# Performance work log

Hardware: AMD Instinct MI355X
Metric: run time of the kernel (lower is better)

## Reference

```python
import jax, jax.numpy as jnp
import numpy as np
import math

N, K, IFZ, AH, AF, QP, VP = 4096, 24, 256, 12, 48, 4, 8


def _rope(x, ang):
    # x: (..., AF), ang: (..., AF//2) rotary angles
    xr = x.reshape(x.shape[:-1] + (AF // 2, 2))
    c, s = jnp.cos(ang), jnp.sin(ang)
    xe, xo = xr[..., 0], xr[..., 1]
    out = jnp.stack([xe * c - xo * s, xe * s + xo * c], axis=-1)
    return out.reshape(x.shape)


def _affine_mul(R, t, vecs):
    # R: (N,3,3), t: (N,3), vecs: (N, ..., 3) -> rigid transform, broadcast over middle dims
    out = jnp.einsum('nij,n...j->n...i', R, vecs)
    return out + t.reshape((t.shape[0],) + (1,) * (vecs.ndim - 2) + (3,))


def setup_inputs():
    key = jax.random.key(0)
    ks = jax.random.split(key, 16)
    sc = 1.0 / math.sqrt(IFZ)
    return {
        'x1': jax.random.normal(ks[0], (N, IFZ), jnp.float32),
        'x2': jax.random.normal(ks[1], (N, K, IFZ // 2), jnp.float32),
        'affines': jax.random.normal(ks[2], (N, 3, 4), jnp.float32),
        'pos_emb': jax.random.normal(ks[3], (N, AF // 2), jnp.float32),
        'edge_index': jax.random.randint(ks[4], (N, K), 0, N),
        'Wq1': jax.random.normal(ks[5], (IFZ, AH * AF), jnp.float32) * sc,
        'Wk1': jax.random.normal(ks[6], (IFZ, AH * AF), jnp.float32) * sc,
        'Wv1': jax.random.normal(ks[7], (IFZ, AH * AF), jnp.float32) * sc,
        'Wq2': jax.random.normal(ks[8], (IFZ, AH * QP * 3), jnp.float32) * sc,
        'Wk2': jax.random.normal(ks[9], (IFZ, AH * QP * 3), jnp.float32) * sc,
        'Wv2': jax.random.normal(ks[10], (IFZ, AH * VP * 3), jnp.float32) * sc,
        'Wbia': jax.random.normal(ks[11], (IFZ // 2, AH), jnp.float32) * (1.0 / math.sqrt(IFZ // 2)),
        'gamma': 1.1 * jnp.ones((1, 1, AH), jnp.float32),
        'Wback': jax.random.normal(ks[12], (AH * AF + AH * (IFZ // 2) + AH * VP * 3 + AH * VP, IFZ), jnp.float32) * 0.02,
        'bback': jnp.zeros((IFZ,), jnp.float32),
        'ln_g': jnp.ones((IFZ,), jnp.float32),
        'ln_b': jnp.zeros((IFZ,), jnp.float32),
    }


def _forward(x1, x2, affines, pos_emb, Wq1, Wk1, Wv1, Wq2, Wk2, Wv2, Wbia, gamma, Wback, bback, ln_g, ln_b, edge_index):
    n = x1.shape[0]
    q1 = (x1 @ Wq1).reshape(n, AH, AF)
    k1 = (x1 @ Wk1).reshape(n, AH, AF)[edge_index]            # (N,K,AH,AF) irregular gather
    q1 = _rope(q1, pos_emb[:, None, :])                       # rotate query by own position
    k1 = _rope(k1, pos_emb[edge_index][:, :, None, :])        # rotate keys by source position
    v1 = (x1 @ Wv1).reshape(n, AH, AF)[edge_index]            # (N,K,AH,AF)
    q2 = (x1 @ Wq2).reshape(n, 1, AH, QP, 3)
    k2 = (x1 @ Wk2).reshape(n, AH, QP, 3)[edge_index]         # (N,K,AH,QP,3)
    v2 = (x1 @ Wv2).reshape(n, AH, VP, 3)
    bias = x2 @ Wbia                                          # (N,K,AH)
    R, t = affines[:, :, :3], affines[:, :, 3]
    wc = math.sqrt(2.0 / (9.0 * QP))
    wl = math.sqrt(1.0 / 3.0)
    s1 = jnp.einsum('nai,nkai->nka', q1, k1) / math.sqrt(AF) + bias
    d = _affine_mul(R, t, q2) - _affine_mul(R, t, k2)         # (N,K,AH,QP,3) point distances
    s2 = -jnp.sum(jnp.square(d), axis=(-1, -2))               # (N,K,AH)
    scores = wl * (s1 + 0.1 * wc * gamma * s2)
    w = jax.nn.softmax(scores, axis=1)                        # softmax over K neighbors
    out1 = jnp.einsum('nka,nkai->nai', w, v1)                 # (N,AH,AF)
    out2 = jnp.einsum('nka,nki->nai', w, x2)                  # (N,AH,IFZ//2)
    v2g = _affine_mul(R, t, v2)[edge_index]                   # transform then gather: (N,K,AH,VP,3)
    oipa = jnp.einsum('nka,nkavd->navd', w, v2g)              # (N,AH,VP,3)
    Rinv = jnp.swapaxes(R, -1, -2)
    tinv = -jnp.einsum('nij,nj->ni', Rinv, t)
    oipa = _affine_mul(Rinv, tinv, oipa)                      # back to local frame
    onorm = jnp.sqrt(jnp.sum(jnp.square(oipa), axis=-1))      # (N,AH,VP)
    cat = jnp.concatenate([out1.reshape(n, -1), out2.reshape(n, -1), oipa.reshape(n, -1), onorm.reshape(n, -1)], axis=1)
    out = cat @ Wback + bback
    h = math.sqrt(2.0) * x1 + out                             # residual with sqrt(2) scale
    mu = jnp.mean(h, axis=-1, keepdims=True)
    var = jnp.var(h, axis=-1, keepdims=True)
    return (h - mu) / jnp.sqrt(var + 1e-5) * ln_g + ln_b


def reference(x1, x2, affines, pos_emb, edge_index, Wq1, Wk1, Wv1, Wq2, Wk2, Wv2, Wbia, gamma, Wback, bback, ln_g, ln_b):
    return _forward(x1, x2, affines, pos_emb, Wq1, Wk1, Wv1, Wq2, Wk2, Wv2, Wbia, gamma, Wback, bback, ln_g, ln_b, edge_index)
```

## Files before the change

kernel.cpp:

```cpp
#include <hip/hip_runtime.h>
#include <hip/hip_bf16.h>
#include <math.h>

#define NN   4096
#define KK   24
#define IFZ  256
#define AH   12
#define AF   48
#define QP   4
#define VP   8

#define TAB_STRIDE 2304
#define Q1OFF 0
#define K1OFF 576
#define V1OFF 1152
#define Q2OFF 1728
#define K2OFF 1872
#define V2OFF 2016

#define CAT_STRIDE 2496
#define CAT_OUT2 576
#define CAT_OIPA 2112
#define CAT_ONRM 2400

#define SPLITK 6

#define WL      0.57735026918962576f
#define C2      0.023570226039551584f
#define RSQRT48 0.14433756729740643f

__global__ __launch_bounds__(256) void pack_w(
    const float* __restrict__ Wq1, const float* __restrict__ Wk1,
    const float* __restrict__ Wv1, const float* __restrict__ Wq2,
    const float* __restrict__ Wk2, const float* __restrict__ Wv2,
    float* __restrict__ packW)
{
    int idx = blockIdx.x * 256 + threadIdx.x;
    int i = idx / TAB_STRIDE;
    int j = idx % TAB_STRIDE;
    float v;
    if (j < 576)       v = Wq1[i*576 + j];
    else if (j < 1152) v = Wk1[i*576 + (j-576)];
    else if (j < 1728) v = Wv1[i*576 + (j-1152)];
    else if (j < 1872) v = Wq2[i*144 + (j-1728)];
    else if (j < 2016) v = Wk2[i*144 + (j-1872)];
    else               v = Wv2[i*288 + (j-2016)];
    packW[idx] = v;
}

__global__ __launch_bounds__(256) void gemm1(
    const float* __restrict__ A, const float* __restrict__ B,
    float* __restrict__ C, int M, int Nc, int Kc)
{
    __shared__ __align__(16) float sA[32][68];
    __shared__ __align__(16) float sB[32][68];
    int bx = blockIdx.x;
    int by = blockIdx.y;
    int tid = threadIdx.x;
    int tx = tid & 15, ty = tid >> 4;
    float acc[4][4] = {};
    for (int k0 = 0; k0 < Kc; k0 += 32) {
        #pragma unroll
        for (int l = 0; l < 2; ++l) {
            int idx = tid + l*256;
            int m = idx >> 3, k4 = (idx & 7) * 4;
            float4 av = *(const float4*)&A[(size_t)(by*64 + m)*Kc + k0 + k4];
            sA[k4+0][m] = av.x; sA[k4+1][m] = av.y;
            sA[k4+2][m] = av.z; sA[k4+3][m] = av.w;
        }
        #pragma unroll
        for (int l = 0; l < 2; ++l) {
            int idx = tid + l*256;
            int kk = idx >> 4, j = (idx & 15) * 4;
            *(float4*)&sB[kk][j] = *(const float4*)&B[(size_t)(k0 + kk)*Nc + bx*64 + j];
        }
        __syncthreads();
        #pragma unroll
        for (int kk = 0; kk < 32; ++kk) {
            float4 a4 = *(const float4*)&sA[kk][ty*4];
            float4 b4 = *(const float4*)&sB[kk][tx*4];
            float a[4] = {a4.x, a4.y, a4.z, a4.w};
            float b[4] = {b4.x, b4.y, b4.z, b4.w};
            #pragma unroll
            for (int u = 0; u < 4; ++u)
                #pragma unroll
                for (int v = 0; v < 4; ++v) acc[u][v] += a[u]*b[v];
        }
        __syncthreads();
    }
    #pragma unroll
    for (int u = 0; u < 4; ++u) {
        float4 o = {acc[u][0], acc[u][1], acc[u][2], acc[u][3]};
        *(float4*)&C[(size_t)(by*64 + ty*4+u)*Nc + bx*64 + tx*4] = o;
    }
}

__global__ __launch_bounds__(256) void gemm3s(
    const float* __restrict__ A, const float* __restrict__ B,
    float* __restrict__ P)
{
    __shared__ __align__(16) float sA[32][68];
    __shared__ __align__(16) float sB[32][68];
    int bx = blockIdx.x;
    int by = blockIdx.y;
    int s  = blockIdx.z;
    int tid = threadIdx.x;
    int tx = tid & 15, ty = tid >> 4;
    const int Kc = CAT_STRIDE, Nc = IFZ;
    float* Pp = P + (size_t)s * NN * IFZ;
    float acc[4][4] = {};
    for (int ki = 0; ki < 13; ++ki) {
        int k0 = s*416 + ki*32;
        #pragma unroll
        for (int l = 0; l < 2; ++l) {
            int idx = tid + l*256;
            int m = idx >> 3, k4 = (idx & 7) * 4;
            float4 av = *(const float4*)&A[(size_t)(by*64 + m)*Kc + k0 + k4];
            sA[k4+0][m] = av.x; sA[k4+1][m] = av.y;
            sA[k4+2][m] = av.z; sA[k4+3][m] = av.w;
        }
        #pragma unroll
        for (int l = 0; l < 2; ++l) {
            int idx = tid + l*256;
            int kk = idx >> 4, j = (idx & 15) * 4;
            *(float4*)&sB[kk][j] = *(const float4*)&B[(size_t)(k0 + kk)*Nc + bx*64 + j];
        }
        __syncthreads();
        #pragma unroll
        for (int kk = 0; kk < 32; ++kk) {
            float4 a4 = *(const float4*)&sA[kk][ty*4];
            float4 b4 = *(const float4*)&sB[kk][tx*4];
            float a[4] = {a4.x, a4.y, a4.z, a4.w};
            float b[4] = {b4.x, b4.y, b4.z, b4.w};
            #pragma unroll
            for (int u = 0; u < 4; ++u)
                #pragma unroll
                for (int v = 0; v < 4; ++v) acc[u][v] += a[u]*b[v];
        }
        __syncthreads();
    }
    #pragma unroll
    for (int u = 0; u < 4; ++u) {
        float4 o = {acc[u][0], acc[u][1], acc[u][2], acc[u][3]};
        *(float4*)&Pp[(size_t)(by*64 + ty*4+u)*Nc + bx*64 + tx*4] = o;
    }
}

__global__ __launch_bounds__(256) void epilogue1(
    float* __restrict__ tab, const float* __restrict__ pos_emb,
    const float* __restrict__ affines)
{
    int node = blockIdx.x * 4 + (threadIdx.x >> 6);
    int lane = threadIdx.x & 63;
    float* row = tab + (size_t)node * TAB_STRIDE;
    const float* pe = pos_emb + node * (AF/2);

    for (int p = lane; p < 576; p += 64) {
        int part = p / 288;
        int pp = p % 288;
        int a = pp / 24, t = pp % 24;
        float ang = pe[t];
        float c = cosf(ang), s = sinf(ang);
        float* b = row + part*576 + a*48 + 2*t;
        float xe = b[0], xo = b[1];
        b[0] = xe*c - xo*s;
        b[1] = xe*s + xo*c;
    }
    float R[9], T[3];
    #pragma unroll
    for (int i = 0; i < 3; ++i) {
        #pragma unroll
        for (int j = 0; j < 3; ++j) R[i*3+j] = affines[node*12 + i*4 + j];
        T[i] = affines[node*12 + i*4 + 3];
    }
    for (int q = lane; q < 144; q += 64) {
        float* b = (q < 48) ? (row + Q2OFF + q*3) : (row + V2OFF + (q-48)*3);
        float x = b[0], y = b[1], z = b[2];
        b[0] = R[0]*x + R[1]*y + R[2]*z + T[0];
        b[1] = R[3]*x + R[4]*y + R[5]*z + T[1];
        b[2] = R[6]*x + R[7]*y + R[8]*z + T[2];
    }
}

__global__ __launch_bounds__(256) void attn_kernel(
    const float* __restrict__ tab, const float* __restrict__ x2,
    const float* __restrict__ affines, const float* __restrict__ Wbia,
    const float* __restrict__ gamma, const int* __restrict__ eidx,
    float* __restrict__ cat)
{
    int n = blockIdx.x;
    int tid = threadIdx.x;

    __shared__ __align__(16) float sQ1[12*52];
    __shared__ __align__(16) float sTq2[144];
    __shared__ __align__(16) float sX2[24*132];
    __shared__ __align__(16) float sWbiaT[12*132];
    __shared__ float sS[288];
    __shared__ float sOipa[288];
    __shared__ float sR[9], sT[3], sG[12];
    __shared__ int   sEoff[24];
    __shared__ float sMax[12], sInv[12];

    const float* row = tab + (size_t)n * TAB_STRIDE;

    for (int j = tid; j < 144; j += 256) {
        int a = j / 12, r = j % 12;
        *(float4*)&sQ1[a*52 + r*4] = *(const float4*)&row[Q1OFF + j*4];
    }
    for (int j = tid; j < 36; j += 256)
        *(float4*)&sTq2[j*4] = *(const float4*)&row[Q2OFF + j*4];
    for (int j = tid; j < 768; j += 256) {
        int k = j >> 5, i4 = j & 31;
        *(float4*)&sX2[k*132 + i4*4] =
            *(const float4*)&x2[(size_t)n*(KK*128) + k*128 + i4*4];
    }
    for (int j = tid; j < 384; j += 256) {
        float4 v = *(const float4*)&Wbia[j*4];
        int base = j*4;
        float tmp[4] = {v.x, v.y, v.z, v.w};
        #pragma unroll
        for (int c = 0; c < 4; ++c) {
            int fl = base + c;
            int i = fl / 12, a = fl - i*12;
            sWbiaT[a*132 + i] = tmp[c];
        }
    }
    if (tid < 9)  sR[tid] = affines[n*12 + (tid/3)*4 + (tid%3)];
    if (tid < 3)  sT[tid] = affines[n*12 + tid*4 + 3];
    if (tid < 12) sG[tid] = gamma[tid];
    if (tid < 24) sEoff[tid] = eidx[n*KK + tid] * TAB_STRIDE;
    __syncthreads();

    for (int j = tid; j < 288; j += 256) {
        int k = j / 12, a = j - k*12;
        const float* krow = tab + sEoff[k];
        const float4* kq4 = (const float4*)(krow + K1OFF + a*48);
        const float4* qq4 = (const float4*)(sQ1 + a*52);
        float s1 = 0.f;
        #pragma unroll
        for (int i = 0; i < 12; ++i) {
            float4 kv = kq4[i], qv = qq4[i];
            s1 += kv.x*qv.x + kv.y*qv.y + kv.z*qv.z + kv.w*qv.w;
        }
        const float4* xr4 = (const float4*)(sX2 + k*132);
        const float4* wr4 = (const float4*)(sWbiaT + a*132);
        float bias = 0.f;
        #pragma unroll 8
        for (int i = 0; i < 32; ++i) {
            float4 xv = xr4[i], wv = wr4[i];
            bias += xv.x*wv.x + xv.y*wv.y + xv.z*wv.z + xv.w*wv.w;
        }
        const float* k2 = krow + K2OFF + a*12;
        float4 k2a = *(const float4*)(k2);
        float4 k2b = *(const float4*)(k2+4);
        float4 k2c = *(const float4*)(k2+8);
        float kx[4] = {k2a.x, k2a.w, k2b.z, k2c.y};
        float ky[4] = {k2a.y, k2b.x, k2b.w, k2c.z};
        float kz[4] = {k2a.z, k2b.y, k2c.x, k2c.w};
        float ss = 0.f;
        #pragma unroll
        for (int p = 0; p < 4; ++p) {
            #pragma unroll
            for (int i = 0; i < 3; ++i) {
                float tk = sR[i*3]*kx[p] + sR[i*3+1]*ky[p] + sR[i*3+2]*kz[p] + sT[i];
                float d = sTq2[a*12 + p*3 + i] - tk;
                ss += d*d;
            }
        }
        sS[j] = WL*(s1*RSQRT48 + bias - C2*sG[a]*ss);
    }
    __syncthreads();
    if (tid < 12) {
        float m = -1e30f;
        for (int k = 0; k < 24; ++k) m = fmaxf(m, sS[k*12 + tid]);
        float s = 0.f;
        for (int k = 0; k < 24; ++k) s += expf(sS[k*12 + tid] - m);
        sMax[tid] = m;
        sInv[tid] = 1.f / s;
    }
    __syncthreads();
    for (int j = tid; j < 288; j += 256) {
        int a = j % 12;
        sS[j] = expf(sS[j] - sMax[a]) * sInv[a];
    }
    __syncthreads();

    float* catRow = cat + (size_t)n * CAT_STRIDE;

    for (int j = tid; j < 216; j += 256) {
        if (j < 144) {
            int a = j / 12;
            float4 acc = {0.f, 0.f, 0.f, 0.f};
            #pragma unroll 6
            for (int k = 0; k < 24; ++k) {
                float w = sS[k*12 + a];
                float4 v = *(const float4*)&tab[sEoff[k] + V1OFF + j*4];
                acc.x += w*v.x; acc.y += w*v.y; acc.z += w*v.z; acc.w += w*v.w;
            }
            *(float4*)&catRow[j*4] = acc;
        } else {
            int j4 = j - 144;
            int a = j4 / 6;
            float4 acc = {0.f, 0.f, 0.f, 0.f};
            #pragma unroll 6
            for (int k = 0; k < 24; ++k) {
                float w = sS[k*12 + a];
                float4 v = *(const float4*)&tab[sEoff[k] + V2OFF + j4*4];
                acc.x += w*v.x; acc.y += w*v.y; acc.z += w*v.z; acc.w += w*v.w;
            }
            *(float4*)&sOipa[j4*4] = acc;
        }
    }
    for (int j = tid; j < 384; j += 256) {
        int a = j >> 5, i4 = j & 31;
        float4 acc = {0.f, 0.f, 0.f, 0.f};
        #pragma unroll 8
        for (int k = 0; k < 24; ++k) {
            float w = sS[k*12 + a];
            float4 v = *(const float4*)&sX2[k*132 + i4*4];
            acc.x += w*v.x; acc.y += w*v.y; acc.z += w*v.z; acc.w += w*v.w;
        }
        *(float4*)&catRow[CAT_OUT2 + j*4] = acc;
    }
    __syncthreads();
    if (tid < 96) {
        int a = tid / 8, p = tid % 8;
        float o0 = sOipa[a*24 + p*3 + 0] - sT[0];
        float o1 = sOipa[a*24 + p*3 + 1] - sT[1];
        float o2 = sOipa[a*24 + p*3 + 2] - sT[2];
        float m0 = sR[0]*o0 + sR[3]*o1 + sR[6]*o2;
        float m1 = sR[1]*o0 + sR[4]*o1 + sR[7]*o2;
        float m2 = sR[2]*o0 + sR[5]*o1 + sR[8]*o2;
        catRow[CAT_OIPA + a*24 + p*3 + 0] = m0;
        catRow[CAT_OIPA + a*24 + p*3 + 1] = m1;
        catRow[CAT_OIPA + a*24 + p*3 + 2] = m2;
        catRow[CAT_ONRM + a*8 + p] = sqrtf(m0*m0 + m1*m1 + m2*m2);
    }
}

__global__ __launch_bounds__(256) void ln_kernel(
    const float* __restrict__ part, const float* __restrict__ x1,
    const float* __restrict__ bback, const float* __restrict__ g,
    const float* __restrict__ b, float* __restrict__ out)
{
    int n = blockIdx.x;
    int tid = threadIdx.x;
    size_t off = (size_t)n*IFZ + tid;
    float h = 1.4142135623730951f * x1[off] + bback[tid];
    #pragma unroll
    for (int s = 0; s < SPLITK; ++s)
        h += part[(size_t)s*NN*IFZ + off];
    float s = h, s2 = h*h;
    #pragma unroll
    for (int off2 = 32; off2 > 0; off2 >>= 1) {
        s  += __shfl_down(s,  off2);
        s2 += __shfl_down(s2, off2);
    }
    __shared__ float ws[4], ws2[4];
    int w = tid >> 6;
    if ((tid & 63) == 0) { ws[w] = s; ws2[w] = s2; }
    __syncthreads();
    float S  = ws[0] + ws[1] + ws[2] + ws[3];
    float S2 = ws2[0] + ws2[1] + ws2[2] + ws2[3];
    float mu = S * (1.f/IFZ);
    float var = S2 * (1.f/IFZ) - mu*mu;
    out[off] = (h - mu) / sqrtf(var + 1e-5f) * g[tid] + b[tid];
}

extern "C" void kernel_launch(void* const* d_in, const int* in_sizes, int n_in,
                              void* d_out, int out_size, void* d_ws, size_t ws_size,
                              hipStream_t stream)
{
    const float* x1      = (const float*)d_in[0];
    const float* x2      = (const float*)d_in[1];
    const float* affines = (const float*)d_in[2];
    const float* pos_emb = (const float*)d_in[3];
    const int*   eidx    = (const int*)  d_in[4];
    const float* Wq1     = (const float*)d_in[5];
    const float* Wk1     = (const float*)d_in[6];
    const float* Wv1     = (const float*)d_in[7];
    const float* Wq2     = (const float*)d_in[8];
    const float* Wk2     = (const float*)d_in[9];
    const float* Wv2     = (const float*)d_in[10];
    const float* Wbia    = (const float*)d_in[11];
    const float* gamma   = (const float*)d_in[12];
    const float* Wback   = (const float*)d_in[13];
    const float* bback   = (const float*)d_in[14];
    const float* ln_g    = (const float*)d_in[15];
    const float* ln_b    = (const float*)d_in[16];
    float* out = (float*)d_out;

    float* ws0 = (float*)d_ws;
    float* packW   = ws0;
    float* nodeTab = packW + (size_t)IFZ*TAB_STRIDE;
    float* catBuf  = nodeTab + (size_t)NN*TAB_STRIDE;
    float* partBuf = nodeTab;

    pack_w<<<(IFZ*TAB_STRIDE)/256, 256, 0, stream>>>(Wq1, Wk1, Wv1, Wq2, Wk2, Wv2, packW);
    gemm1<<<dim3(TAB_STRIDE/64, NN/64), 256, 0, stream>>>(x1, packW, nodeTab, NN, TAB_STRIDE, IFZ);
    epilogue1<<<NN/4, 256, 0, stream>>>(nodeTab, pos_emb, affines);
    attn_kernel<<<NN, 256, 0, stream>>>(nodeTab, x2, affines, Wbia, gamma, eidx, catBuf);
    gemm3s<<<dim3(IFZ/64, NN/64, SPLITK), 256, 0, stream>>>(catBuf, Wback, partBuf);
    ln_kernel<<<NN, 256, 0, stream>>>(partBuf, x1, bback, ln_g, ln_b, out);
}
```

Before: 411.0 us.

## Precompute pair bias in a separate kernel and cache rope sin/cos

Moves the x2·Wbia pair-bias computation out of the attention kernel into a dedicated bias_kernel that writes a per-node 288-entry buffer, which attn_kernel then loads instead of transposing Wbia and running 32-step dot products per (k, head). The rope epilogue computes cos/sin once per angle into shared memory rather than once per element. Unroll factors on the value-gather loops are also changed. This adds an extra kernel launch, reads x2 one more time, and uses extra workspace, in exchange for a lighter attention kernel with less shared memory and less serial work per thread.

```diff
diff --git a/kernel.cpp b/kernel.cpp
--- a/kernel.cpp
+++ b/kernel.cpp
@@ -146,21 +146,59 @@
     }
 }
 
+__global__ __launch_bounds__(384) void bias_kernel(
+    const float* __restrict__ x2, const float* __restrict__ Wbia,
+    float* __restrict__ biasOut)
+{
+    __shared__ __align__(16) float sWT[12*132];
+    int tid = threadIdx.x;
+    {
+        float4 v = *(const float4*)&Wbia[tid*4];
+        int base = tid*4;
+        float tmp[4] = {v.x, v.y, v.z, v.w};
+        #pragma unroll
+        for (int c = 0; c < 4; ++c) {
+            int fl = base + c;
+            int i = fl / 12, a = fl - i*12;
+            sWT[a*132 + i] = tmp[c];
+        }
+    }
+    __syncthreads();
+    int r_local = tid / 12, a = tid - r_local*12;
+    size_t row = (size_t)blockIdx.x*32 + r_local;
+    const float4* xr = (const float4*)&x2[row*128];
+    const float4* wr = (const float4*)&sWT[a*132];
+    float acc = 0.f;
+    #pragma unroll 8
+    for (int i = 0; i < 32; ++i) {
+        float4 xv = xr[i], wv = wr[i];
+        acc += xv.x*wv.x + xv.y*wv.y + xv.z*wv.z + xv.w*wv.w;
+    }
+    biasOut[row*12 + a] = acc;
+}
+
 __global__ __launch_bounds__(256) void epilogue1(
     float* __restrict__ tab, const float* __restrict__ pos_emb,
     const float* __restrict__ affines)
 {
-    int node = blockIdx.x * 4 + (threadIdx.x >> 6);
+    __shared__ float sC[4][24], sSn[4][24];
+    int wv   = threadIdx.x >> 6;
+    int node = blockIdx.x * 4 + wv;
     int lane = threadIdx.x & 63;
     float* row = tab + (size_t)node * TAB_STRIDE;
-    const float* pe = pos_emb + node * (AF/2);
+
+    if (lane < 24) {
+        float ang = pos_emb[node*24 + lane];
+        sC[wv][lane]  = cosf(ang);
+        sSn[wv][lane] = sinf(ang);
+    }
+    __syncthreads();
 
     for (int p = lane; p < 576; p += 64) {
         int part = p / 288;
         int pp = p % 288;
         int a = pp / 24, t = pp % 24;
-        float ang = pe[t];
-        float c = cosf(ang), s = sinf(ang);
+        float c = sC[wv][t], s = sSn[wv][t];
         float* b = row + part*576 + a*48 + 2*t;
         float xe = b[0], xo = b[1];
         b[0] = xe*c - xo*s;
@@ -184,7 +222,7 @@
 
 __global__ __launch_bounds__(256) void attn_kernel(
     const float* __restrict__ tab, const float* __restrict__ x2,
-    const float* __restrict__ affines, const float* __restrict__ Wbia,
+    const float* __restrict__ affines, const float* __restrict__ biasIn,
     const float* __restrict__ gamma, const int* __restrict__ eidx,
     float* __restrict__ cat)
 {
@@ -194,7 +232,7 @@
     __shared__ __align__(16) float sQ1[12*52];
     __shared__ __align__(16) float sTq2[144];
     __shared__ __align__(16) float sX2[24*132];
-    __shared__ __align__(16) float sWbiaT[12*132];
+    __shared__ __align__(16) float sBias[288];
     __shared__ float sS[288];
     __shared__ float sOipa[288];
     __shared__ float sR[9], sT[3], sG[12];
@@ -214,17 +252,8 @@
         *(float4*)&sX2[k*132 + i4*4] =
             *(const float4*)&x2[(size_t)n*(KK*128) + k*128 + i4*4];
     }
-    for (int j = tid; j < 384; j += 256) {
-        float4 v = *(const float4*)&Wbia[j*4];
-        int base = j*4;
-        float tmp[4] = {v.x, v.y, v.z, v.w};
-        #pragma unroll
-        for (int c = 0; c < 4; ++c) {
-            int fl = base + c;
-            int i = fl / 12, a = fl - i*12;
-            sWbiaT[a*132 + i] = tmp[c];
-        }
-    }
+    for (int j = tid; j < 72; j += 256)
+        *(float4*)&sBias[j*4] = *(const float4*)&biasIn[(size_t)n*288 + j*4];
     if (tid < 9)  sR[tid] = affines[n*12 + (tid/3)*4 + (tid%3)];
     if (tid < 3)  sT[tid] = affines[n*12 + tid*4 + 3];
     if (tid < 12) sG[tid] = gamma[tid];
@@ -241,14 +270,6 @@
         for (int i = 0; i < 12; ++i) {
             float4 kv = kq4[i], qv = qq4[i];
             s1 += kv.x*qv.x + kv.y*qv.y + kv.z*qv.z + kv.w*qv.w;
-        }
-        const float4* xr4 = (const float4*)(sX2 + k*132);
-        const float4* wr4 = (const float4*)(sWbiaT + a*132);
-        float bias = 0.f;
-        #pragma unroll 8
-        for (int i = 0; i < 32; ++i) {
-            float4 xv = xr4[i], wv = wr4[i];
-            bias += xv.x*wv.x + xv.y*wv.y + xv.z*wv.z + xv.w*wv.w;
         }
         const float* k2 = krow + K2OFF + a*12;
         float4 k2a = *(const float4*)(k2);
@@ -267,7 +288,7 @@
                 ss += d*d;
             }
         }
-        sS[j] = WL*(s1*RSQRT48 + bias - C2*sG[a]*ss);
+        sS[j] = WL*(s1*RSQRT48 + sBias[j] - C2*sG[a]*ss);
     }
     __syncthreads();
     if (tid < 12) {
@@ -291,7 +312,7 @@
         if (j < 144) {
             int a = j / 12;
             float4 acc = {0.f, 0.f, 0.f, 0.f};
-            #pragma unroll 6
+            #pragma unroll 8
             for (int k = 0; k < 24; ++k) {
                 float w = sS[k*12 + a];
                 float4 v = *(const float4*)&tab[sEoff[k] + V1OFF + j*4];
@@ -302,7 +323,7 @@
             int j4 = j - 144;
             int a = j4 / 6;
             float4 acc = {0.f, 0.f, 0.f, 0.f};
-            #pragma unroll 6
+            #pragma unroll 8
             for (int k = 0; k < 24; ++k) {
                 float w = sS[k*12 + a];
                 float4 v = *(const float4*)&tab[sEoff[k] + V2OFF + j4*4];
@@ -394,12 +415,14 @@
     float* packW   = ws0;
     float* nodeTab = packW + (size_t)IFZ*TAB_STRIDE;
     float* catBuf  = nodeTab + (size_t)NN*TAB_STRIDE;
+    float* biasBuf = catBuf + (size_t)NN*CAT_STRIDE;
     float* partBuf = nodeTab;
 
     pack_w<<<(IFZ*TAB_STRIDE)/256, 256, 0, stream>>>(Wq1, Wk1, Wv1, Wq2, Wk2, Wv2, packW);
+    bias_kernel<<<(NN*KK)/32, 384, 0, stream>>>(x2, Wbia, biasBuf);
     gemm1<<<dim3(TAB_STRIDE/64, NN/64), 256, 0, stream>>>(x1, packW, nodeTab, NN, TAB_STRIDE, IFZ);
     epilogue1<<<NN/4, 256, 0, stream>>>(nodeTab, pos_emb, affines);
-    attn_kernel<<<NN, 256, 0, stream>>>(nodeTab, x2, affines, Wbia, gamma, eidx, catBuf);
+    attn_kernel<<<NN, 256, 0, stream>>>(nodeTab, x2, affines, biasBuf, gamma, eidx, catBuf);
     gemm3s<<<dim3(IFZ/64, NN/64, SPLITK), 256, 0, stream>>>(catBuf, Wback, partBuf);
     ln_kernel<<<NN, 256, 0, stream>>>(partBuf, x1, bback, ln_g, ln_b, out);
 }
```

Measured after the change: 386.5 us. 6.0% less time.
